# Kernel tuning notes

Hardware: AMD Instinct MI355X
Metric: run time of the kernel (lower is better)

The kernel has to match this reference:

```python
import jax, jax.numpy as jnp
import numpy as np

ALPHA = 1.0  # softness coefficient


def _soft_assign(data, centroids):
    # data: (B, N, D), centroids: (B, K, D)
    # squared euclidean distance -> (B, N, K)
    dist = jnp.sum((data[:, :, None, :] - centroids[:, None, :, :]) ** 2, axis=-1)
    return jax.nn.softmax(-ALPHA * dist, axis=2)


def _update_once(data, probs):
    # weighted centroid update: (B, K, D)
    denom = jnp.sum(probs, axis=1)  # (B, K)
    centroids = jnp.einsum('bnk,bnd->bkd', probs, data) / denom[:, :, None]
    probs = _soft_assign(data, centroids)
    return probs, centroids


def setup_inputs() -> dict:
    key = jax.random.key(0)
    k1, k2 = jax.random.split(key)
    B, N, D, K = 8, 65536, 40, 2
    data = jax.random.normal(k1, (B, N, D), dtype=jnp.float32)
    centroid_ids = jax.random.randint(k2, (B, K), 0, N)
    return {"data": data, "centroid_ids": centroid_ids, "iteration": 10}


def reference(data, centroid_ids, iteration):
    # init centroids by gathering selected samples (random init path)
    centroids = jnp.take_along_axis(data, centroid_ids[:, :, None], axis=1)  # (B, K, D)
    probs = _soft_assign(data, centroids)

    def body(i, carry):
        probs, _ = carry
        return _update_once(data, probs)

    probs, centroids = jax.lax.fori_loop(0, iteration, body, (probs, centroids))
    return probs
```

## Files before the change

### kernel.cpp

```cpp
#include <hip/hip_runtime.h>
#include <hip/hip_fp16.h>
#include <cstddef>

#define BB    8
#define NN    65536
#define DD    40
#define NITER 10

#define PREPB  128
#define PTPB   256
#define PTILES 2
#define PADF4  11
#define PBLK   64
#define TPB    512
#define CHUNKS 2
#define ROW    44


__device__ __forceinline__ float rfl(float x) {
    return __int_as_float(__builtin_amdgcn_readfirstlane(__float_as_int(x)));
}
__device__ __forceinline__ float prob0(float diff) {
    return __builtin_amdgcn_rcpf(1.f + __expf(diff));
}

__device__ __forceinline__ void gh_from_ids(const float* __restrict__ data,
                                            const int* __restrict__ ids, int b,
                                            float gs[DD], float& hs, int tid) {
    __shared__ float gbuf[DD], sqbuf[DD], hbuf;
    if (tid < DD) {
        const int i0 = ids[b * 2 + 0];
        const int i1 = ids[b * 2 + 1];
        const float c0 = data[((size_t)b * NN + i0) * DD + tid];
        const float c1 = data[((size_t)b * NN + i1) * DD + tid];
        gbuf[tid]  = c0 - c1;
        sqbuf[tid] = c0 * c0 - c1 * c1;
    }
    __syncthreads();
    if (tid == 0) {
        float h = 0.f;
#pragma unroll
        for (int i = 0; i < DD; ++i) h += sqbuf[i];
        hbuf = h;
    }
    __syncthreads();
#pragma unroll
    for (int i = 0; i < DD; ++i) gs[i] = rfl(gbuf[i]);
    hs = rfl(hbuf);
    __syncthreads();
}

template <int ROWS>
__device__ __forceinline__ void gh_from_partials(const float* __restrict__ pp,
                                                 const float* __restrict__ S, int b,
                                                 float gs[DD], float& hs, int tid) {
    __shared__ float part[41][8];
    __shared__ float red[41], gbuf[DD], sqbuf[DD], hbuf;
    if (tid < 328) {
        const int v = tid % 41, q = tid / 41;
        const float* base = pp + (size_t)b * ROWS * ROW;
        float s = 0.f;
#pragma unroll
        for (int j = 0; j < ROWS / 8; ++j)
            s += base[(size_t)(q * (ROWS / 8) + j) * ROW + v];
        part[v][q] = s;
    }
    __syncthreads();
    if (tid < 41) {
        float s = 0.f;
#pragma unroll
        for (int q = 0; q < 8; ++q) s += part[tid][q];
        red[tid] = s;
    }
    __syncthreads();
    if (tid < DD) {
        const float num = red[tid], den = red[DD];
        const float c0 = num / den;
        const float c1 = (S[b * DD + tid] - num) / ((float)NN - den);
        gbuf[tid]  = c0 - c1;
        sqbuf[tid] = c0 * c0 - c1 * c1;
    }
    __syncthreads();
    if (tid == 0) {
        float h = 0.f;
#pragma unroll
        for (int i = 0; i < DD; ++i) h += sqbuf[i];
        hbuf = h;
    }
    __syncthreads();
#pragma unroll
    for (int i = 0; i < DD; ++i) gs[i] = rfl(gbuf[i]);
    hs = rfl(hbuf);
    __syncthreads();
}


__global__ __launch_bounds__(PTPB, 3) void k_prep(const float* __restrict__ data,
                                                  const int* __restrict__ ids,
                                                  __half2* __restrict__ dataT,
                                                  float* __restrict__ psOut,
                                                  float* __restrict__ ppOut) {
    const int pb = blockIdx.x, b = blockIdx.y, tid = threadIdx.x;
    __shared__ float4 stg[PTPB * PADF4];

    float gs[DD], hs;
    gh_from_ids(data, ids, b, gs, hs, tid);

    float vals[2 * DD + 1];
#pragma unroll
    for (int i = 0; i <= 2 * DD; ++i) vals[i] = 0.f;

#pragma unroll
    for (int t = 0; t < PTILES; ++t) {
        const int basePt = pb * (PTPB * PTILES) + t * PTPB;
        const float4* src = (const float4*)(data + ((size_t)b * NN + basePt) * DD);
        __syncthreads();
#pragma unroll
        for (int j = 0; j < 10; ++j) {
            const unsigned f = tid + j * PTPB;
            stg[(f / 10u) * PADF4 + (f % 10u)] = src[f];
        }
        __syncthreads();
        float4 xv[10];
#pragma unroll
        for (int c = 0; c < 10; ++c) xv[c] = stg[tid * PADF4 + c];

        float a0 = 0.f, a1 = 0.f, a2 = 0.f, a3 = 0.f;
#pragma unroll
        for (int c = 0; c < 10; ++c) {
            vals[41 + 4 * c + 0] += xv[c].x; vals[41 + 4 * c + 1] += xv[c].y;
            vals[41 + 4 * c + 2] += xv[c].z; vals[41 + 4 * c + 3] += xv[c].w;
            a0 = fmaf(xv[c].x, gs[4 * c + 0], a0);
            a1 = fmaf(xv[c].y, gs[4 * c + 1], a1);
            a2 = fmaf(xv[c].z, gs[4 * c + 2], a2);
            a3 = fmaf(xv[c].w, gs[4 * c + 3], a3);
        }
        const float p0 = prob0(fmaf(-2.f, (a0 + a1) + (a2 + a3), hs));
        vals[DD] += p0;
#pragma unroll
        for (int c = 0; c < 10; ++c) {
            vals[4 * c + 0] = fmaf(p0, xv[c].x, vals[4 * c + 0]);
            vals[4 * c + 1] = fmaf(p0, xv[c].y, vals[4 * c + 1]);
            vals[4 * c + 2] = fmaf(p0, xv[c].z, vals[4 * c + 2]);
            vals[4 * c + 3] = fmaf(p0, xv[c].w, vals[4 * c + 3]);
        }
        __half2* dst = dataT + (size_t)b * (DD / 2) * NN + basePt + tid;
#pragma unroll
        for (int c = 0; c < 10; ++c) {
            dst[(size_t)(2 * c + 0) * NN] = __floats2half2_rn(xv[c].x, xv[c].y);
            dst[(size_t)(2 * c + 1) * NN] = __floats2half2_rn(xv[c].z, xv[c].w);
        }
    }

#pragma unroll
    for (int i = 0; i <= 2 * DD; ++i) {
        vals[i] += __shfl_xor(vals[i], 32, 64);
        vals[i] += __shfl_xor(vals[i], 16, 64);
    }
    float* rbuf = (float*)stg;
    __shared__ float part2[2 * DD + 1][2];
    __syncthreads();
    const int lane = tid & 63, wave = tid >> 6;
    if (lane < 16) {
        const int row = wave * 16 + lane;
#pragma unroll
        for (int i = 0; i <= 2 * DD; ++i) rbuf[row * 84 + i] = vals[i];
    }
    __syncthreads();
    if (tid < 162) {
        const int v = tid % 81, q = tid / 81;
        float s = 0.f;
#pragma unroll 8
        for (int j = 0; j < 32; ++j) s += rbuf[(q * 32 + j) * 84 + v];
        part2[v][q] = s;
    }
    __syncthreads();
    if (tid < 81) {
        const float s = part2[tid][0] + part2[tid][1];
        if (tid < 41) ppOut[(size_t)(b * PREPB + pb) * ROW + tid] = s;
        else          psOut[(size_t)(b * PREPB + pb) * 40 + (tid - 41)] = s;
    }
}

__global__ void k_reduceS(const float* __restrict__ psIn, float* __restrict__ S) {
    const int tid = threadIdx.x;
    __shared__ float tmp[BB * DD][2];
    const int i = tid >> 1, half = tid & 1;
    if (i < BB * DD) {
        const int b = i / DD, d = i % DD;
        float s = 0.f;
#pragma unroll 8
        for (int r = 0; r < PREPB / 2; ++r)
            s += psIn[(size_t)(b * PREPB + half * (PREPB / 2) + r) * 40 + d];
        tmp[i][half] = s;
    }
    __syncthreads();
    if (i < BB * DD && half == 0) S[i] = tmp[i][0] + tmp[i][1];
}

template <int MODE, int ROWS>
__global__ __launch_bounds__(TPB, 2) void k_pass(const __half2* __restrict__ dataT,
                                                 const float* __restrict__ ppIn,
                                                 const float* __restrict__ S,
                                                 float* __restrict__ ppOut,
                                                 float* __restrict__ out) {
    const int pb = blockIdx.x, b = blockIdx.y, tid = threadIdx.x;

    float gs[DD], hs;
    gh_from_partials<ROWS>(ppIn, S, b, gs, hs, tid);

    float acc[DD + 1];
    if constexpr (MODE == 1) {
#pragma unroll
        for (int i = 0; i <= DD; ++i) acc[i] = 0.f;
    }

    const __half2* colBase = dataT + (size_t)b * (DD / 2) * NN;

#pragma unroll
    for (int ch = 0; ch < CHUNKS; ++ch) {
        const int n0 = pb * (TPB * CHUNKS) + ch * TPB + tid;
        const __half2* p = colBase + n0;
        float x[DD];
        float a0 = 0.f, a1 = 0.f, a2 = 0.f, a3 = 0.f;
#pragma unroll
        for (int dp = 0; dp < DD / 2; ++dp) {
            const float2 v = __half22float2(p[(size_t)dp * NN]);
            x[2 * dp] = v.x; x[2 * dp + 1] = v.y;
            if (dp & 1) {
                a2 = fmaf(v.x, gs[2 * dp], a2);
                a3 = fmaf(v.y, gs[2 * dp + 1], a3);
            } else {
                a0 = fmaf(v.x, gs[2 * dp], a0);
                a1 = fmaf(v.y, gs[2 * dp + 1], a1);
            }
        }
        const float p0 = prob0(fmaf(-2.f, (a0 + a1) + (a2 + a3), hs));

        if constexpr (MODE == 2) {
            ((float2*)out)[(size_t)b * NN + n0] = make_float2(p0, 1.f - p0);
        } else {
            acc[DD] += p0;
#pragma unroll
            for (int d = 0; d < DD; ++d) acc[d] = fmaf(p0, x[d], acc[d]);
        }
    }

    if constexpr (MODE == 1) {
#pragma unroll
        for (int i = 0; i <= DD; ++i) {
            acc[i] += __shfl_xor(acc[i], 32, 64);
            acc[i] += __shfl_xor(acc[i], 16, 64);
        }
        __shared__ float rbuf[128 * ROW];
        __shared__ float part2[DD + 1][8];
        const int lane = tid & 63, wave = tid >> 6;
        if (lane < 16) {
            const int row = wave * 16 + lane;
#pragma unroll
            for (int i = 0; i <= DD; ++i) rbuf[row * ROW + i] = acc[i];
        }
        __syncthreads();
        if (tid < 328) {
            const int v = tid % 41, q = tid / 41;
            float s = 0.f;
#pragma unroll
            for (int j = 0; j < 16; ++j) s += rbuf[(q * 16 + j) * ROW + v];
            part2[v][q] = s;
        }
        __syncthreads();
        if (tid <= DD) {
            float s = 0.f;
#pragma unroll
            for (int q = 0; q < 8; ++q) s += part2[tid][q];
            ppOut[(size_t)(b * PBLK + pb) * ROW + tid] = s;
        }
    }
}


extern "C" void kernel_launch(void* const* d_in, const int* in_sizes, int n_in,
                              void* d_out, int out_size, void* d_ws, size_t ws_size,
                              hipStream_t stream) {
    const float* data = (const float*)d_in[0];
    const int*   ids  = (const int*)d_in[1];

    float* ws      = (float*)d_ws;
    __half2* dataT = (__half2*)ws;
    float* after   = ws + (size_t)BB * (DD / 2) * NN;
    float* pA      = after;
    float* pp1     = pA + (size_t)BB * PREPB * ROW;
    float* pp2     = pp1 + (size_t)BB * PBLK * ROW;
    float* pS      = pp2 + (size_t)BB * PBLK * ROW;
    float* S       = pS + (size_t)BB * PREPB * 40;
    float* out     = (float*)d_out;

    k_prep<<<dim3(PREPB, BB), PTPB, 0, stream>>>(data, ids, dataT, pS, pA);
    k_reduceS<<<1, 640, 0, stream>>>(pS, S);

    const dim3 grid(PBLK, BB);
    k_pass<1, PREPB><<<grid, TPB, 0, stream>>>(dataT, pA, S, pp1, nullptr);
    const float* cur = pp1;
    float* nxt = pp2;
    for (int t = 0; t < NITER - 2; ++t) {
        k_pass<1, PBLK><<<grid, TPB, 0, stream>>>(dataT, cur, S, nxt, nullptr);
        const float* tmp = cur; cur = nxt; nxt = (float*)tmp;
    }
    k_pass<2, PBLK><<<grid, TPB, 0, stream>>>(dataT, cur, S, nullptr, out);
}
```

Baseline: 146.6 us.

## Process two points per thread with 8-byte loads and halve prep staging

The pass kernel now handles two adjacent points per thread using a single 8-byte load per dimension pair, with 256-thread blocks and a 128-block grid per batch. This replaces the 512-thread, two-chunk scheme. The prep kernel stages fp16 instead of fp32 in shared memory and reuses the same half values for the transposed store and the moments, which lowers LDS use and allows higher occupancy. Partial-reduction sizes are unified to 128 rows. This adds more global reads of partials per block and raises register pressure from holding two points' data.

```diff
diff --git a/kernel.cpp b/kernel.cpp
--- a/kernel.cpp
+++ b/kernel.cpp
@@ -10,10 +10,9 @@
 #define PREPB  128
 #define PTPB   256
 #define PTILES 2
-#define PADF4  11
-#define PBLK   64
-#define TPB    512
-#define CHUNKS 2
+#define PSTR   22
+#define PBLK   128
+#define TPB    256
 #define ROW    44
 
 
@@ -50,28 +49,23 @@
     __syncthreads();
 }
 
-template <int ROWS>
 __device__ __forceinline__ void gh_from_partials(const float* __restrict__ pp,
                                                  const float* __restrict__ S, int b,
                                                  float gs[DD], float& hs, int tid) {
-    __shared__ float part[41][8];
+    __shared__ float part[41][4];
     __shared__ float red[41], gbuf[DD], sqbuf[DD], hbuf;
-    if (tid < 328) {
+    if (tid < 164) {
         const int v = tid % 41, q = tid / 41;
-        const float* base = pp + (size_t)b * ROWS * ROW;
+        const float* base = pp + (size_t)b * PREPB * ROW;
         float s = 0.f;
-#pragma unroll
-        for (int j = 0; j < ROWS / 8; ++j)
-            s += base[(size_t)(q * (ROWS / 8) + j) * ROW + v];
+#pragma unroll 8
+        for (int j = 0; j < 32; ++j)
+            s += base[(size_t)(q * 32 + j) * ROW + v];
         part[v][q] = s;
     }
     __syncthreads();
-    if (tid < 41) {
-        float s = 0.f;
-#pragma unroll
-        for (int q = 0; q < 8; ++q) s += part[tid][q];
-        red[tid] = s;
-    }
+    if (tid < 41)
+        red[tid] = (part[tid][0] + part[tid][1]) + (part[tid][2] + part[tid][3]);
     __syncthreads();
     if (tid < DD) {
         const float num = red[tid], den = red[DD];
@@ -95,13 +89,14 @@
 }
 
 
-__global__ __launch_bounds__(PTPB, 3) void k_prep(const float* __restrict__ data,
+__global__ __launch_bounds__(PTPB, 4) void k_prep(const float* __restrict__ data,
                                                   const int* __restrict__ ids,
                                                   __half2* __restrict__ dataT,
                                                   float* __restrict__ psOut,
                                                   float* __restrict__ ppOut) {
     const int pb = blockIdx.x, b = blockIdx.y, tid = threadIdx.x;
-    __shared__ float4 stg[PTPB * PADF4];
+    __shared__ unsigned stg[PTPB * PSTR];
+    __half2* stgh = (__half2*)stg;
 
     float gs[DD], hs;
     gh_from_ids(data, ids, b, gs, hs, tid);
@@ -118,38 +113,35 @@
 #pragma unroll
         for (int j = 0; j < 10; ++j) {
             const unsigned f = tid + j * PTPB;
-            stg[(f / 10u) * PADF4 + (f % 10u)] = src[f];
-        }
-        __syncthreads();
-        float4 xv[10];
-#pragma unroll
-        for (int c = 0; c < 10; ++c) xv[c] = stg[tid * PADF4 + c];
+            const float4 v = src[f];
+            const unsigned slot = (f / 10u) * PSTR + (f % 10u) * 2u;
+            stgh[slot]     = __floats2half2_rn(v.x, v.y);
+            stgh[slot + 1] = __floats2half2_rn(v.z, v.w);
+        }
+        __syncthreads();
+        __half2 xh[20];
+        const __half2* rp = stgh + tid * PSTR;
+#pragma unroll
+        for (int q = 0; q < 20; ++q) xh[q] = rp[q];
+
+        __half2* dst = dataT + (size_t)b * (DD / 2) * NN + basePt + tid;
+#pragma unroll
+        for (int q = 0; q < 20; ++q) dst[(size_t)q * NN] = xh[q];
 
         float a0 = 0.f, a1 = 0.f, a2 = 0.f, a3 = 0.f;
-#pragma unroll
-        for (int c = 0; c < 10; ++c) {
-            vals[41 + 4 * c + 0] += xv[c].x; vals[41 + 4 * c + 1] += xv[c].y;
-            vals[41 + 4 * c + 2] += xv[c].z; vals[41 + 4 * c + 3] += xv[c].w;
-            a0 = fmaf(xv[c].x, gs[4 * c + 0], a0);
-            a1 = fmaf(xv[c].y, gs[4 * c + 1], a1);
-            a2 = fmaf(xv[c].z, gs[4 * c + 2], a2);
-            a3 = fmaf(xv[c].w, gs[4 * c + 3], a3);
+        float x[DD];
+#pragma unroll
+        for (int q = 0; q < 20; ++q) {
+            const float2 v = __half22float2(xh[q]);
+            x[2 * q] = v.x; x[2 * q + 1] = v.y;
+            vals[41 + 2 * q] += v.x; vals[41 + 2 * q + 1] += v.y;
+            if (q & 1) { a2 = fmaf(v.x, gs[2 * q], a2); a3 = fmaf(v.y, gs[2 * q + 1], a3); }
+            else       { a0 = fmaf(v.x, gs[2 * q], a0); a1 = fmaf(v.y, gs[2 * q + 1], a1); }
         }
         const float p0 = prob0(fmaf(-2.f, (a0 + a1) + (a2 + a3), hs));
         vals[DD] += p0;
 #pragma unroll
-        for (int c = 0; c < 10; ++c) {
-            vals[4 * c + 0] = fmaf(p0, xv[c].x, vals[4 * c + 0]);
-            vals[4 * c + 1] = fmaf(p0, xv[c].y, vals[4 * c + 1]);
-            vals[4 * c + 2] = fmaf(p0, xv[c].z, vals[4 * c + 2]);
-            vals[4 * c + 3] = fmaf(p0, xv[c].w, vals[4 * c + 3]);
-        }
-        __half2* dst = dataT + (size_t)b * (DD / 2) * NN + basePt + tid;
-#pragma unroll
-        for (int c = 0; c < 10; ++c) {
-            dst[(size_t)(2 * c + 0) * NN] = __floats2half2_rn(xv[c].x, xv[c].y);
-            dst[(size_t)(2 * c + 1) * NN] = __floats2half2_rn(xv[c].z, xv[c].w);
-        }
+        for (int d = 0; d < DD; ++d) vals[d] = fmaf(p0, x[d], vals[d]);
     }
 
 #pragma unroll
@@ -198,8 +190,8 @@
     if (i < BB * DD && half == 0) S[i] = tmp[i][0] + tmp[i][1];
 }
 
-template <int MODE, int ROWS>
-__global__ __launch_bounds__(TPB, 2) void k_pass(const __half2* __restrict__ dataT,
+template <int MODE>
+__global__ __launch_bounds__(TPB, 3) void k_pass(const __half2* __restrict__ dataT,
                                                  const float* __restrict__ ppIn,
                                                  const float* __restrict__ S,
                                                  float* __restrict__ ppOut,
@@ -207,7 +199,7 @@
     const int pb = blockIdx.x, b = blockIdx.y, tid = threadIdx.x;
 
     float gs[DD], hs;
-    gh_from_partials<ROWS>(ppIn, S, b, gs, hs, tid);
+    gh_from_partials(ppIn, S, b, gs, hs, tid);
 
     float acc[DD + 1];
     if constexpr (MODE == 1) {
@@ -215,45 +207,40 @@
         for (int i = 0; i <= DD; ++i) acc[i] = 0.f;
     }
 
-    const __half2* colBase = dataT + (size_t)b * (DD / 2) * NN;
-
-#pragma unroll
-    for (int ch = 0; ch < CHUNKS; ++ch) {
-        const int n0 = pb * (TPB * CHUNKS) + ch * TPB + tid;
-        const __half2* p = colBase + n0;
-        float x[DD];
-        float a0 = 0.f, a1 = 0.f, a2 = 0.f, a3 = 0.f;
-#pragma unroll
-        for (int dp = 0; dp < DD / 2; ++dp) {
-            const float2 v = __half22float2(p[(size_t)dp * NN]);
-            x[2 * dp] = v.x; x[2 * dp + 1] = v.y;
-            if (dp & 1) {
-                a2 = fmaf(v.x, gs[2 * dp], a2);
-                a3 = fmaf(v.y, gs[2 * dp + 1], a3);
-            } else {
-                a0 = fmaf(v.x, gs[2 * dp], a0);
-                a1 = fmaf(v.y, gs[2 * dp + 1], a1);
-            }
-        }
-        const float p0 = prob0(fmaf(-2.f, (a0 + a1) + (a2 + a3), hs));
-
-        if constexpr (MODE == 2) {
-            ((float2*)out)[(size_t)b * NN + n0] = make_float2(p0, 1.f - p0);
-        } else {
-            acc[DD] += p0;
-#pragma unroll
-            for (int d = 0; d < DD; ++d) acc[d] = fmaf(p0, x[d], acc[d]);
-        }
-    }
-
-    if constexpr (MODE == 1) {
+    const int n0 = pb * (TPB * 2) + tid * 2;
+    const __half2* p = dataT + (size_t)b * (DD / 2) * NN + n0;
+
+    float xa[DD], xb[DD];
+    float da0 = 0.f, da1 = 0.f, db0 = 0.f, db1 = 0.f;
+#pragma unroll
+    for (int dp = 0; dp < DD / 2; ++dp) {
+        const uint2 u = *(const uint2*)(p + (size_t)dp * NN);
+        const float2 va = __half22float2(*(const __half2*)&u.x);
+        const float2 vb = __half22float2(*(const __half2*)&u.y);
+        xa[2 * dp] = va.x; xa[2 * dp + 1] = va.y;
+        xb[2 * dp] = vb.x; xb[2 * dp + 1] = vb.y;
+        da0 = fmaf(va.x, gs[2 * dp], da0); da1 = fmaf(va.y, gs[2 * dp + 1], da1);
+        db0 = fmaf(vb.x, gs[2 * dp], db0); db1 = fmaf(vb.y, gs[2 * dp + 1], db1);
+    }
+    const float p0a = prob0(fmaf(-2.f, da0 + da1, hs));
+    const float p0b = prob0(fmaf(-2.f, db0 + db1, hs));
+
+    if constexpr (MODE == 2) {
+        *(float4*)(out + ((size_t)b * NN + n0) * 2) =
+            make_float4(p0a, 1.f - p0a, p0b, 1.f - p0b);
+    } else {
+        acc[DD] += p0a + p0b;
+#pragma unroll
+        for (int d = 0; d < DD; ++d)
+            acc[d] = fmaf(p0a, xa[d], fmaf(p0b, xb[d], acc[d]));
+
 #pragma unroll
         for (int i = 0; i <= DD; ++i) {
             acc[i] += __shfl_xor(acc[i], 32, 64);
             acc[i] += __shfl_xor(acc[i], 16, 64);
         }
-        __shared__ float rbuf[128 * ROW];
-        __shared__ float part2[DD + 1][8];
+        __shared__ float rbuf[64 * ROW];
+        __shared__ float part2[DD + 1][4];
         const int lane = tid & 63, wave = tid >> 6;
         if (lane < 16) {
             const int row = wave * 16 + lane;
@@ -261,7 +248,7 @@
             for (int i = 0; i <= DD; ++i) rbuf[row * ROW + i] = acc[i];
         }
         __syncthreads();
-        if (tid < 328) {
+        if (tid < 164) {
             const int v = tid % 41, q = tid / 41;
             float s = 0.f;
 #pragma unroll
@@ -269,12 +256,9 @@
             part2[v][q] = s;
         }
         __syncthreads();
-        if (tid <= DD) {
-            float s = 0.f;
-#pragma unroll
-            for (int q = 0; q < 8; ++q) s += part2[tid][q];
-            ppOut[(size_t)(b * PBLK + pb) * ROW + tid] = s;
-        }
+        if (tid <= DD)
+            ppOut[(size_t)(b * PBLK + pb) * ROW + tid] =
+                (part2[tid][0] + part2[tid][1]) + (part2[tid][2] + part2[tid][3]);
     }
 }
 
@@ -290,8 +274,8 @@
     float* after   = ws + (size_t)BB * (DD / 2) * NN;
     float* pA      = after;
     float* pp1     = pA + (size_t)BB * PREPB * ROW;
-    float* pp2     = pp1 + (size_t)BB * PBLK * ROW;
-    float* pS      = pp2 + (size_t)BB * PBLK * ROW;
+    float* pp2     = pp1 + (size_t)BB * PREPB * ROW;
+    float* pS      = pp2 + (size_t)BB * PREPB * ROW;
     float* S       = pS + (size_t)BB * PREPB * 40;
     float* out     = (float*)d_out;
 
@@ -299,12 +283,12 @@
     k_reduceS<<<1, 640, 0, stream>>>(pS, S);
 
     const dim3 grid(PBLK, BB);
-    k_pass<1, PREPB><<<grid, TPB, 0, stream>>>(dataT, pA, S, pp1, nullptr);
+    k_pass<1><<<grid, TPB, 0, stream>>>(dataT, pA, S, pp1, nullptr);
     const float* cur = pp1;
     float* nxt = pp2;
     for (int t = 0; t < NITER - 2; ++t) {
-        k_pass<1, PBLK><<<grid, TPB, 0, stream>>>(dataT, cur, S, nxt, nullptr);
+        k_pass<1><<<grid, TPB, 0, stream>>>(dataT, cur, S, nxt, nullptr);
         const float* tmp = cur; cur = nxt; nxt = (float*)tmp;
     }
-    k_pass<2, PBLK><<<grid, TPB, 0, stream>>>(dataT, cur, S, nullptr, out);
-}
+    k_pass<2><<<grid, TPB, 0, stream>>>(dataT, cur, S, nullptr, out);
+}
```

Result: slower. 162.2 us (+10.7%).
